# Optimization experiments

Measured on AMD Instinct MI355X. Metric: run time of the kernel, lower is better.

Reference implementation:

```python
import jax, jax.numpy as jnp
import numpy as np
from jax import lax

FS = 48000.0
PI = 3.14159265358979323846

def bilinear_low_shelf(fc, gain_db, Q, fs):
    A = 10.0 ** (gain_db / 40.0)
    w0 = 2.0 * PI * fc / fs
    alpha = jnp.sin(w0) / (2.0 * Q)
    cosw = jnp.cos(w0)
    sqA = jnp.sqrt(A)
    b0 = A * (A + 1 - (A - 1) * cosw + 2 * sqA * alpha)
    b1 = 2 * A * (A - 1 - (A + 1) * cosw)
    b2 = A * (A + 1 - (A - 1) * cosw - 2 * sqA * alpha)
    a0 = A + 1 + (A - 1) * cosw + 2 * sqA * alpha
    a1 = -2 * (A - 1 + (A + 1) * cosw)
    a2 = A + 1 + (A - 1) * cosw - 2 * sqA * alpha
    return (b0 / a0, b1 / a0, b2 / a0, a1 / a0, a2 / a0)

def biquad(x, b0, b1, b2, a1, a2):
    # x: [B, T]; direct-form-II-transposed biquad with zero initial state
    B = x.shape[0]
    z0 = (jnp.zeros((B,), x.dtype), jnp.zeros((B,), x.dtype))
    def step(carry, xn):
        z1, z2 = carry
        yn = b0 * xn + z1
        z1n = b1 * xn - a1 * yn + z2
        z2n = b2 * xn - a2 * yn
        return (z1n, z2n), yn
    _, yT = lax.scan(step, z0, x.T)  # scan over time axis
    return yT.T

def setup_inputs() -> dict:
    key = jax.random.key(0)
    x = jax.random.normal(key, (64, 480000), dtype=jnp.float32)
    return {
        "x": x,
        "low_gain_db": jnp.float32(6.0),
        "mid_gain_db": jnp.float32(-3.0),
        "mid_fc": jnp.float32(800.0),
        "mid_Q": jnp.float32(1.0),
        "high_gain_db": jnp.float32(4.0),
    }

def reference(x, low_gain_db, mid_gain_db, mid_fc, mid_Q, high_gain_db):
    c = bilinear_low_shelf(jnp.float32(120.0), low_gain_db, jnp.float32(0.707), FS)
    y = biquad(x, *c)
    c = bilinear_low_shelf(mid_fc, mid_gain_db, mid_Q, FS)
    y = biquad(y, *c)
    c = bilinear_low_shelf(jnp.float32(4000.0), high_gain_db, jnp.float32(0.707), FS)
    y = biquad(y, *c)
    return y
```

## Files before the change

kernel.cpp:

```cpp
#include <hip/hip_runtime.h>
#include <math.h>


constexpr int T_LEN  = 480000;
constexpr int B_ROWS = 64;
constexpr int CHUNK  = 64;
constexpr int LOG2C  = 6;
constexpr int KCH    = T_LEN / CHUNK;
constexpr int NT     = 256;
constexpr int HISTC  = 21;
constexpr int MTERM  = 21;
constexpr int OUTC   = NT - HISTC;
constexpr int BLKROW = (KCH + OUTC - 1) / OUTC;
constexpr int NBLK   = B_ROWS * BLKROW;
constexpr int NWAVE  = NT / 64;

struct Coeffs { float b0, b1, b2, a1, a2; };

__device__ __forceinline__ float rfl(float v) {
    return __int_as_float(__builtin_amdgcn_readfirstlane(__float_as_int(v)));
}

__device__ __forceinline__ Coeffs shelf(float fc, float gdb, float Q) {
    float A  = powf(10.0f, gdb * (1.0f / 40.0f));
    float w0 = 2.0f * 3.14159265358979323846f * fc / 48000.0f;
    float sw = sinf(w0), cw = cosf(w0);
    float alpha = sw / (2.0f * Q);
    float sqA = sqrtf(A);
    float b0 = A * ((A + 1.0f) - (A - 1.0f) * cw + 2.0f * sqA * alpha);
    float b1 = 2.0f * A * ((A - 1.0f) - (A + 1.0f) * cw);
    float b2 = A * ((A + 1.0f) - (A - 1.0f) * cw - 2.0f * sqA * alpha);
    float a0 = (A + 1.0f) + (A - 1.0f) * cw + 2.0f * sqA * alpha;
    float a1 = -2.0f * ((A - 1.0f) + (A + 1.0f) * cw);
    float a2 = (A + 1.0f) + (A - 1.0f) * cw - 2.0f * sqA * alpha;
    float rr = 1.0f / a0;
    Coeffs c;
    c.b0 = rfl(b0 * rr); c.b1 = rfl(b1 * rr); c.b2 = rfl(b2 * rr);
    c.a1 = rfl(a1 * rr); c.a2 = rfl(a2 * rr);
    return c;
}

__device__ __forceinline__ float bq(float xn, const Coeffs& c, float& z1, float& z2) {
    float y = fmaf(c.b0, xn, z1);
    z1 = fmaf(-c.a1, y, fmaf(c.b1, xn, z2));
    z2 = fmaf(c.b2, xn, -(c.a2 * y));
    return y;
}

__device__ __forceinline__ float step6(float s[6], float x,
                                       const Coeffs& c1, const Coeffs& c2, const Coeffs& c3) {
    float y1 = bq(x,  c1, s[0], s[1]);
    float y2 = bq(y1, c2, s[2], s[3]);
    float y3 = bq(y2, c3, s[4], s[5]);
    return y3;
}

__device__ __forceinline__ float corr(float y0, const float* cnp, const float t6[6]) {
    float4 ca = *(const float4*)(cnp);
    float2 cb = *(const float2*)(cnp + 4);
    float acc = fmaf(ca.x, t6[0], y0);
    acc = fmaf(ca.y, t6[1], acc);
    acc = fmaf(ca.z, t6[2], acc);
    acc = fmaf(ca.w, t6[3], acc);
    acc = fmaf(cb.x, t6[4], acc);
    acc = fmaf(cb.y, t6[5], acc);
    return acc;
}

__global__ __launch_bounds__(256, 4) void k_fused(
    const float* __restrict__ x,
    const float* __restrict__ p_lg, const float* __restrict__ p_mg,
    const float* __restrict__ p_mf, const float* __restrict__ p_mq,
    const float* __restrict__ p_hg,
    float* __restrict__ out)
{
    __shared__ __align__(16) float smem[4096];
    __shared__ float M[36];
    __shared__ float Pw[LOG2C * 36];
    __shared__ float Crow[8];
    __shared__ __align__(16) float cn[64 * 8];

    const int t = threadIdx.x;
    const int r = blockIdx.x / BLKROW;
    const int b = blockIdx.x - r * BLKROW;
    const int c = b * OUTC + t - HISTC;
    const bool active = (c >= 0) && (c < KCH);

    Coeffs c1 = shelf(120.0f,  *p_lg, 0.707f);
    Coeffs c2 = shelf(*p_mf,   *p_mg, *p_mq);
    Coeffs c3 = shelf(4000.0f, *p_hg, 0.707f);

    float4 xv[16];
    {
        int cc = c < 0 ? 0 : c;
        const float4* lp = (const float4*)(x + (long long)r * T_LEN + (long long)cc * CHUNK);
        if (active) {
            #pragma unroll
            for (int q = 0; q < 16; ++q) xv[q] = lp[q];
        } else {
            #pragma unroll
            for (int q = 0; q < 16; ++q) xv[q] = make_float4(0.f, 0.f, 0.f, 0.f);
        }
    }

    float s[6] = {0.f, 0.f, 0.f, 0.f, 0.f, 0.f};
    #pragma unroll
    for (int q = 0; q < 16; ++q) {
        float4 v = xv[q];
        v.x = step6(s, v.x, c1, c2, c3);
        v.y = step6(s, v.y, c1, c2, c3);
        v.z = step6(s, v.z, c1, c2, c3);
        v.w = step6(s, v.w, c1, c2, c3);
        xv[q] = v;
    }
    #pragma unroll
    for (int i = 0; i < 6; ++i) smem[t * 7 + i] = s[i];

    if (t < 6) {
        float e[6] = {0.f, 0.f, 0.f, 0.f, 0.f, 0.f};
        e[t] = 1.0f;
        float y = step6(e, 0.0f, c1, c2, c3);
        #pragma unroll
        for (int i = 0; i < 6; ++i) M[i * 6 + t] = e[i];
        Crow[t] = y;
    }
    __syncthreads();

    for (int it = 0; it < LOG2C; ++it) {
        float acc = 0.f;
        if (t < 36) {
            Pw[it * 36 + t] = M[t];
            int i = t / 6, j = t - 6 * (t / 6);
            #pragma unroll
            for (int q = 0; q < 6; ++q) acc = fmaf(M[i * 6 + q], M[q * 6 + j], acc);
        }
        __syncthreads();
        if (t < 36) M[t] = acc;
        __syncthreads();
    }
    float a[36];
    #pragma unroll
    for (int i = 0; i < 36; ++i) a[i] = rfl(M[i]);

    if (t < 64) {
        float row[6];
        #pragma unroll
        for (int j = 0; j < 6; ++j) row[j] = Crow[j];
        for (int k = 0; k < LOG2C; ++k) {
            if ((t >> k) & 1) {
                const float* P = Pw + k * 36;
                float nr[6];
                #pragma unroll
                for (int j = 0; j < 6; ++j) {
                    float acc = 0.f;
                    #pragma unroll
                    for (int q = 0; q < 6; ++q) acc = fmaf(row[q], P[q * 6 + j], acc);
                    nr[j] = acc;
                }
                #pragma unroll
                for (int j = 0; j < 6; ++j) row[j] = nr[j];
            }
        }
        #pragma unroll
        for (int j = 0; j < 6; ++j) cn[t * 8 + j] = row[j];
    }

    float t6[6] = {0.f, 0.f, 0.f, 0.f, 0.f, 0.f};
    int m0 = t - MTERM; if (m0 < 0) m0 = 0;
    for (int m = m0; m < t; ++m) {
        float dm[6];
        #pragma unroll
        for (int i = 0; i < 6; ++i) dm[i] = smem[m * 7 + i];
        float nt6[6];
        #pragma unroll
        for (int i = 0; i < 6; ++i) {
            float acc = dm[i];
            #pragma unroll
            for (int j = 0; j < 6; ++j) acc = fmaf(a[i * 6 + j], t6[j], acc);
            nt6[i] = acc;
        }
        #pragma unroll
        for (int i = 0; i < 6; ++i) t6[i] = nt6[i];
    }

    __syncthreads();

    #pragma unroll
    for (int q = 0; q < 16; ++q) {
        float4 v = xv[q];
        v.x = corr(v.x, cn + (4 * q + 0) * 8, t6);
        v.y = corr(v.y, cn + (4 * q + 1) * 8, t6);
        v.z = corr(v.z, cn + (4 * q + 2) * 8, t6);
        v.w = corr(v.w, cn + (4 * q + 3) * 8, t6);
        xv[q] = v;
    }

    float4* sv = (float4*)smem;
    const int slot = t & 63;
    const int wv   = t >> 6;
    float4* op = (float4*)(out + (long long)r * T_LEN);
    for (int rr = 0; rr < NWAVE; ++rr) {
        if (wv == rr) {
            #pragma unroll
            for (int q = 0; q < 16; ++q) {
                int byte = (slot * 256 + q * 16) ^ ((slot & 7) << 4);
                sv[byte >> 4] = xv[q];
            }
        }
        __syncthreads();
        const int chunkBase = b * OUTC + 64 * rr - HISTC;
        #pragma unroll
        for (int j = 0; j < 4; ++j) {
            int f  = 256 * j + t;
            int aa = f >> 4;
            int qq = f & 15;
            int tr = 64 * rr + aa;
            int cc = chunkBase + aa;
            if (tr >= HISTC && cc < KCH) {
                int byte = (aa * 256 + qq * 16) ^ ((aa & 7) << 4);
                op[(long long)cc * 16 + qq] = sv[byte >> 4];
            }
        }
        __syncthreads();
    }
}

extern "C" void kernel_launch(void* const* d_in, const int* in_sizes, int n_in,
                              void* d_out, int out_size, void* d_ws, size_t ws_size,
                              hipStream_t stream) {
    const float* x  = (const float*)d_in[0];
    const float* lg = (const float*)d_in[1];
    const float* mg = (const float*)d_in[2];
    const float* mf = (const float*)d_in[3];
    const float* mq = (const float*)d_in[4];
    const float* hg = (const float*)d_in[5];
    float* out = (float*)d_out;

    hipLaunchKernelGGL(k_fused, dim3(NBLK), dim3(NT), 0, stream,
                       x, lg, mg, mf, mq, hg, out);
}
```

Before: 232.6 us.

## Cut block barriers: wave-local matrix powers, per-wave output transpose, shorter history

Wave 0 now computes the 6x6 transition matrix powers with cross-lane shuffles instead of shared memory and multiple __syncthreads rounds. It overlaps this with the chunk filtering done by the other waves. The output staging becomes a per-wave transpose through private shared-memory slices, which removes the block-wide barriers in the store loop. The halo history drops from 21 to 17 chunks and occupancy hints rise to 6 blocks, so less redundant halo work is done, at the risk of a less accurate state reconstruction and register spills.

Result: slower. 285.9 us (+22.9%).

```diff
diff --git a/kernel.cpp b/kernel.cpp
--- a/kernel.cpp
+++ b/kernel.cpp
@@ -8,12 +8,11 @@
 constexpr int LOG2C  = 6;
 constexpr int KCH    = T_LEN / CHUNK;
 constexpr int NT     = 256;
-constexpr int HISTC  = 21;
-constexpr int MTERM  = 21;
+constexpr int HISTC  = 17;
+constexpr int MTERM  = 17;
 constexpr int OUTC   = NT - HISTC;
 constexpr int BLKROW = (KCH + OUTC - 1) / OUTC;
 constexpr int NBLK   = B_ROWS * BLKROW;
-constexpr int NWAVE  = NT / 64;
 
 struct Coeffs { float b0, b1, b2, a1, a2; };
 
@@ -67,7 +66,7 @@
     return acc;
 }
 
-__global__ __launch_bounds__(256, 4) void k_fused(
+__global__ __launch_bounds__(256, 6) void k_fused(
     const float* __restrict__ x,
     const float* __restrict__ p_lg, const float* __restrict__ p_mg,
     const float* __restrict__ p_mf, const float* __restrict__ p_mq,
@@ -80,10 +79,13 @@
     __shared__ float Crow[8];
     __shared__ __align__(16) float cn[64 * 8];
 
-    const int t = threadIdx.x;
+    const int t    = threadIdx.x;
+    const int lane = t & 63;
+    const int w    = t >> 6;
     const int r = blockIdx.x / BLKROW;
     const int b = blockIdx.x - r * BLKROW;
     const int c = b * OUTC + t - HISTC;
+    const int cbase = b * OUTC - HISTC;
     const bool active = (c >= 0) && (c < KCH);
 
     Coeffs c1 = shelf(120.0f,  *p_lg, 0.707f);
@@ -101,6 +103,31 @@
             #pragma unroll
             for (int q = 0; q < 16; ++q) xv[q] = make_float4(0.f, 0.f, 0.f, 0.f);
         }
+    }
+
+    if (w == 0) {
+        const int i  = lane / 6;
+        const int j  = lane - 6 * i;
+        const int i6 = i * 6;
+        float e[6];
+        #pragma unroll
+        for (int jj = 0; jj < 6; ++jj) e[jj] = (jj == j) ? 1.0f : 0.0f;
+        float y = step6(e, 0.0f, c1, c2, c3);
+        if (lane < 6) Crow[lane] = y;
+        float aM = e[0];
+        #pragma unroll
+        for (int ii = 1; ii < 6; ++ii) aM = (i == ii) ? e[ii] : aM;
+        for (int it = 0; it < LOG2C; ++it) {
+            if (lane < 36) Pw[it * 36 + lane] = aM;
+            float acc = 0.f;
+            #pragma unroll
+            for (int q = 0; q < 6; ++q) {
+                int sA = i6 + q; if (sA > 63) sA = 63;
+                acc = fmaf(__shfl(aM, sA, 64), __shfl(aM, q * 6 + j, 64), acc);
+            }
+            aM = acc;
+        }
+        if (lane < 36) M[lane] = aM;
     }
 
     float s[6] = {0.f, 0.f, 0.f, 0.f, 0.f, 0.f};
@@ -116,53 +143,34 @@
     #pragma unroll
     for (int i = 0; i < 6; ++i) smem[t * 7 + i] = s[i];
 
-    if (t < 6) {
-        float e[6] = {0.f, 0.f, 0.f, 0.f, 0.f, 0.f};
-        e[t] = 1.0f;
-        float y = step6(e, 0.0f, c1, c2, c3);
-        #pragma unroll
-        for (int i = 0; i < 6; ++i) M[i * 6 + t] = e[i];
-        Crow[t] = y;
-    }
     __syncthreads();
 
-    for (int it = 0; it < LOG2C; ++it) {
-        float acc = 0.f;
-        if (t < 36) {
-            Pw[it * 36 + t] = M[t];
-            int i = t / 6, j = t - 6 * (t / 6);
-            #pragma unroll
-            for (int q = 0; q < 6; ++q) acc = fmaf(M[i * 6 + q], M[q * 6 + j], acc);
-        }
-        __syncthreads();
-        if (t < 36) M[t] = acc;
-        __syncthreads();
-    }
     float a[36];
     #pragma unroll
     for (int i = 0; i < 36; ++i) a[i] = rfl(M[i]);
 
-    if (t < 64) {
+    if (w == 1) {
         float row[6];
         #pragma unroll
-        for (int j = 0; j < 6; ++j) row[j] = Crow[j];
+        for (int jj = 0; jj < 6; ++jj) row[jj] = Crow[jj];
+        #pragma unroll
         for (int k = 0; k < LOG2C; ++k) {
-            if ((t >> k) & 1) {
+            if ((lane >> k) & 1) {
                 const float* P = Pw + k * 36;
                 float nr[6];
                 #pragma unroll
-                for (int j = 0; j < 6; ++j) {
+                for (int jj = 0; jj < 6; ++jj) {
                     float acc = 0.f;
                     #pragma unroll
-                    for (int q = 0; q < 6; ++q) acc = fmaf(row[q], P[q * 6 + j], acc);
-                    nr[j] = acc;
+                    for (int q = 0; q < 6; ++q) acc = fmaf(row[q], P[q * 6 + jj], acc);
+                    nr[jj] = acc;
                 }
                 #pragma unroll
-                for (int j = 0; j < 6; ++j) row[j] = nr[j];
+                for (int jj = 0; jj < 6; ++jj) row[jj] = nr[jj];
             }
         }
         #pragma unroll
-        for (int j = 0; j < 6; ++j) cn[t * 8 + j] = row[j];
+        for (int jj = 0; jj < 6; ++jj) cn[lane * 8 + jj] = row[jj];
     }
 
     float t6[6] = {0.f, 0.f, 0.f, 0.f, 0.f, 0.f};
@@ -195,33 +203,28 @@
         xv[q] = v;
     }
 
-    float4* sv = (float4*)smem;
-    const int slot = t & 63;
-    const int wv   = t >> 6;
+    float4* qv = ((float4*)smem) + w * 256;
     float4* op = (float4*)(out + (long long)r * T_LEN);
-    for (int rr = 0; rr < NWAVE; ++rr) {
-        if (wv == rr) {
-            #pragma unroll
-            for (int q = 0; q < 16; ++q) {
-                int byte = (slot * 256 + q * 16) ^ ((slot & 7) << 4);
-                sv[byte >> 4] = xv[q];
+    #pragma unroll
+    for (int j = 0; j < 4; ++j) {
+        if ((lane >> 4) == j) {
+            const int sl  = lane & 15;
+            const int key = sl & 7;
+            #pragma unroll
+            for (int q = 0; q < 16; ++q)
+                qv[sl * 16 + (q ^ key)] = xv[q];
+        }
+        const long long base4 = (long long)(cbase + w * 64 + 16 * j) * 16;
+        #pragma unroll
+        for (int i = 0; i < 4; ++i) {
+            const int sl = i * 4 + (lane >> 4);
+            const int qq = lane & 15;
+            const int tr = w * 64 + 16 * j + sl;
+            const int cc = cbase + tr;
+            if (tr >= HISTC && cc < KCH) {
+                op[base4 + i * 64 + lane] = qv[sl * 16 + (qq ^ (sl & 7))];
             }
         }
-        __syncthreads();
-        const int chunkBase = b * OUTC + 64 * rr - HISTC;
-        #pragma unroll
-        for (int j = 0; j < 4; ++j) {
-            int f  = 256 * j + t;
-            int aa = f >> 4;
-            int qq = f & 15;
-            int tr = 64 * rr + aa;
-            int cc = chunkBase + aa;
-            if (tr >= HISTC && cc < KCH) {
-                int byte = (aa * 256 + qq * 16) ^ ((aa & 7) << 4);
-                op[(long long)cc * 16 + qq] = sv[byte >> 4];
-            }
-        }
-        __syncthreads();
     }
 }
 
```
